# Kernel optimization log

Hardware: AMD Instinct MI355X
Metric: run time of the kernel (lower is better)

The kernel has to match this reference:

```python
import jax, jax.numpy as jnp
import numpy as np

N = 50000     # nodes
E = 800000    # edges (avg degree 16)
IN = 128
HID = 128
OUT = 128


def _init_lin(key, n_out, n_in, bias=True):
    k1, k2 = jax.random.split(key)
    bound = 1.0 / np.sqrt(n_in)
    W = jax.random.uniform(k1, (n_out, n_in), minval=-bound, maxval=bound, dtype=jnp.float32)
    if bias:
        b = jax.random.uniform(k2, (n_out,), minval=-bound, maxval=bound, dtype=jnp.float32)
        return W, b
    return W


def setup_inputs() -> dict:
    key = jax.random.key(0)
    ks = jax.random.split(key, 20)
    inp = {
        "s": jax.random.normal(ks[0], (N, IN), dtype=jnp.float32),
        "t": jax.random.normal(ks[1], (N, IN), dtype=jnp.float32),
        "edge_index": jax.random.randint(ks[2], (2, E), 0, N, dtype=jnp.int64),
        "edge_weight": jax.random.normal(ks[3], (E,), dtype=jnp.float32),
    }
    dims = [(HID, IN), (OUT, HID)]
    i = 4
    for layer in range(2):
        n_out, n_in = dims[layer]
        for pre in ("s", "t"):
            Wl, bl = _init_lin(ks[i], n_out, n_in, bias=True); i += 1
            Wr = _init_lin(ks[i], n_out, n_in, bias=False); i += 1
            inp[f"{pre}{layer}_Wl"] = Wl
            inp[f"{pre}{layer}_bl"] = bl
            inp[f"{pre}{layer}_Wr"] = Wr
    return inp


def _sage(x, src, dst, w, Wl, bl, Wr):
    """SAGEConv (mean aggr, weighted messages): lin_l(mean_j w_ij x_j) + lin_r(x_i)."""
    n = x.shape[0]
    msg = x[src] * w[:, None]                                   # [E, d] gather
    agg = jax.ops.segment_sum(msg, dst, num_segments=n)         # [N, d] scatter-add
    cnt = jax.ops.segment_sum(jnp.ones_like(w), dst, num_segments=n)
    mean = agg / jnp.maximum(cnt, 1.0)[:, None]
    return mean @ Wl.T + bl + x @ Wr.T


def reference(s, t, edge_index, edge_weight,
              s0_Wl, s0_bl, s0_Wr, t0_Wl, t0_bl, t0_Wr,
              s1_Wl, s1_bl, s1_Wr, t1_Wl, t1_bl, t1_Wr):
    w = jax.nn.sigmoid(edge_weight)
    src, dst = edge_index[0], edge_index[1]
    # layer 0 (relu; dropout is identity in eval mode)
    s1 = jax.nn.relu(_sage(t, src, dst, w, s0_Wl, s0_bl, s0_Wr))
    t1 = jax.nn.relu(_sage(s, dst, src, w, t0_Wl, t0_bl, t0_Wr))  # flipped edges
    # layer 1 (no activation)
    s2 = _sage(t1, src, dst, w, s1_Wl, s1_bl, s1_Wr)
    t2 = _sage(s1, dst, src, w, t1_Wl, t1_bl, t1_Wr)
    return (s2, t2)
```

## Files before the change

kernel.cpp:

```cpp
#include <hip/hip_runtime.h>
#include <hip/hip_bf16.h>

#define DIM 128
#define BINSHIFT 8
#define BINSZ 256
#define MAXBINS2 400
#define EPB 2048
#define CAP 6144

typedef __attribute__((ext_vector_type(4))) float f32x4;
typedef __attribute__((ext_vector_type(8))) _Float16 h16x8;
typedef __attribute__((ext_vector_type(2))) _Float16 h16x2;
typedef __attribute__((ext_vector_type(8))) unsigned short u16x8;

static __device__ __forceinline__ unsigned short f2h(float f) {
    _Float16 h = (_Float16)f;
    return __builtin_bit_cast(unsigned short, h);
}

#if __has_builtin(__builtin_amdgcn_fdot2)
static __device__ __forceinline__ float dot2(h16x2 a, h16x2 b, float c) {
    return __builtin_amdgcn_fdot2(a, b, c, false);
}
#else
static __device__ __forceinline__ float dot2(h16x2 a, h16x2 b, float c) {
    return c + (float)a.x * (float)b.x + (float)a.y * (float)b.y;
}
#endif

struct WPtrs { const float* Wl[4]; const float* Wr[4]; };

__global__ __launch_bounds__(256) void dgnn_prep(
        const float* __restrict__ s, const float* __restrict__ t,
        unsigned short* __restrict__ sb, unsigned short* __restrict__ tb,
        int n4, int cvtb, WPtrs wp, unsigned short* __restrict__ Wc, int wbase,
        int* __restrict__ binCur, int nb2) {
    int b = blockIdx.x;
    if (b < wbase) {
        int which = (b >= cvtb) ? 1 : 0;
        int i = (b - which * cvtb) * 256 + threadIdx.x;
        if (i >= n4) return;
        const float* src = which ? t : s;
        unsigned short* dst = which ? tb : sb;
        float4 v = ((const float4*)src)[i];
        ushort4 o;
        o.x = f2h(v.x); o.y = f2h(v.y); o.z = f2h(v.z); o.w = f2h(v.w);
        ((ushort4*)dst)[i] = o;
    } else if (b < wbase + 128) {
        int tid = (b - wbase) * 256 + threadIdx.x;
        int i4 = tid << 2;
        int conv = i4 >> 15;
        int rem = i4 & 32767;
        int ch = rem >> 8;
        int k = rem & 255;
        const float* src = (k < 128) ? wp.Wl[conv] : wp.Wr[conv];
        float4 v = *(const float4*)(src + ch * DIM + (k & 127));
        ushort4 o;
        o.x = f2h(v.x); o.y = f2h(v.y); o.z = f2h(v.z); o.w = f2h(v.w);
        *(ushort4*)(Wc + i4) = o;
    } else {
        for (int i = threadIdx.x; i < nb2; i += 256) binCur[i] = 0;
    }
}

__global__ __launch_bounds__(256) void dgnn_binscatter(const float* __restrict__ ew,
        const int* __restrict__ srcI, const int* __restrict__ dstI,
        int* __restrict__ binCur, int2* __restrict__ binned, int E, int NBINS) {
    __shared__ int hist[MAXBINS2];
    const int nb2 = 2 * NBINS;
    for (int i = threadIdx.x; i < nb2; i += 256) hist[i] = 0;
    __syncthreads();
    int base = blockIdx.x * EPB;
    int end = min(base + EPB, E);
    for (int e = base + threadIdx.x; e < end; e += 256) {
        atomicAdd(&hist[dstI[e] >> BINSHIFT], 1);
        atomicAdd(&hist[NBINS + (srcI[e] >> BINSHIFT)], 1);
    }
    __syncthreads();
    for (int i = threadIdx.x; i < nb2; i += 256) {
        int c = hist[i];
        int st = c ? atomicAdd(&binCur[i], c) : 0;
        hist[i] = i * CAP + st;
    }
    __syncthreads();
    for (int e = base + threadIdx.x; e < end; e += 256) {
        int d = dstI[e], s = srcI[e];
        float x = ew[e];
        float w = 1.0f / (1.0f + expf(-x));
        int wb = __float_as_int(w);
        int packed = d | (s << 16);
        int pd = atomicAdd(&hist[d >> BINSHIFT], 1);
        binned[pd] = make_int2(packed, wb);
        int ps = atomicAdd(&hist[NBINS + (s >> BINSHIFT)], 1);
        binned[ps] = make_int2(packed, wb);
    }
}

__global__ __launch_bounds__(256) void dgnn_csrfinal(const int2* __restrict__ binned,
        const int* __restrict__ binCur,
        int* __restrict__ offsD, int* __restrict__ degD,
        int* __restrict__ offsS, int* __restrict__ degS,
        unsigned int* __restrict__ nbrPD, unsigned int* __restrict__ nbrPS,
        int N, int NBINS) {
    int b = blockIdx.x;
    bool isD = b < NBINS;
    int lb = isD ? b : b - NBINS;
    int nodeBase = lb << BINSHIFT;
    const int2* bin = binned + (size_t)b * CAP;
    int K = binCur[b]; if (K > CAP) K = CAP;
    int* offs = isD ? offsD : offsS;
    int* dga  = isD ? degD : degS;
    unsigned int* out = (isD ? nbrPD : nbrPS) + (size_t)lb * CAP;

    __shared__ int cnt[BINSZ], cur[BINSZ], scanb[BINSZ];
    cnt[threadIdx.x] = 0;
    __syncthreads();
    for (int i = threadIdx.x; i < K; i += 256) {
        int pk = bin[i].x;
        int node = isD ? (pk & 0xffff) : ((pk >> 16) & 0xffff);
        atomicAdd(&cnt[node - nodeBase], 1);
    }
    __syncthreads();
    int v = cnt[threadIdx.x];
    scanb[threadIdx.x] = v;
    __syncthreads();
#pragma unroll
    for (int o = 1; o < 256; o <<= 1) {
        int u = (threadIdx.x >= o) ? scanb[threadIdx.x - o] : 0;
        __syncthreads();
        scanb[threadIdx.x] += u;
        __syncthreads();
    }
    int pos = scanb[threadIdx.x] - v;
    cur[threadIdx.x] = pos;
    int n = nodeBase + threadIdx.x;
    if (n < N) { offs[n] = lb * CAP + pos; dga[n] = v; }
    __syncthreads();
    for (int i = threadIdx.x; i < K; i += 256) {
        int2 en = bin[i];
        int node, nbr;
        if (isD) { node = en.x & 0xffff; nbr = (en.x >> 16) & 0xffff; }
        else     { node = (en.x >> 16) & 0xffff; nbr = en.x & 0xffff; }
        int p = atomicAdd(&cur[node - nodeBase], 1);
        unsigned short wh = f2h(__int_as_float(en.y));
        out[p] = (unsigned int)nbr | ((unsigned int)wh << 16);
    }
}

__global__ __launch_bounds__(256, 8) void dgnn_gather2(
        const unsigned short* __restrict__ xbD, const int* __restrict__ offsD,
        const int* __restrict__ degD, const unsigned int* __restrict__ nbrD,
        unsigned short* __restrict__ meanD,
        const unsigned short* __restrict__ xbS, const int* __restrict__ offsS,
        const int* __restrict__ degS, const unsigned int* __restrict__ nbrS,
        unsigned short* __restrict__ meanS,
        int N, int halfb) {
    int which = (blockIdx.x >= halfb) ? 1 : 0;
    const unsigned short* xb = which ? xbS : xbD;
    const int* offs          = which ? offsS : offsD;
    const int* dga           = which ? degS : degD;
    const unsigned int* nbrP = which ? nbrS : nbrD;
    unsigned short* meanb    = which ? meanS : meanD;

    long long gid = (long long)(blockIdx.x - which * halfb) * 256 + threadIdx.x;
    int n = (int)(gid >> 5);
    if (n >= N) return;
    const int l32 = (int)gid & 31;
    const int q2  = l32 >> 4;
    const int m   = l32 & 15;

    int beg = offs[n];
    int dg  = dga[n];
    int end = beg + dg;
    float acc[8];
#pragma unroll
    for (int k = 0; k < 8; k++) acc[k] = 0.f;

    for (int base = beg; base < end; base += 32) {
        int cnt = end - base; if (cnt > 32) cnt = 32;
        bool inb = (base + l32) < end;
        unsigned int pk_l = inb ? nbrP[base + l32] : 0u;

        for (int it = 0; it < cnt; it += 16) {
            int e0 = it + (q2 << 1);
            unsigned int p[8];
#pragma unroll
            for (int j = 0; j < 4; j++) {
                p[2 * j]     = __shfl(pk_l, e0 + 4 * j, 32);
                p[2 * j + 1] = __shfl(pk_l, e0 + 4 * j + 1, 32);
            }
            uint4 v[8];
#pragma unroll
            for (int j = 0; j < 8; j++)
                v[j] = *(const uint4*)(xb + ((size_t)(p[j] & 0xffffu) << 7) + (m << 3));
#pragma unroll
            for (int j = 0; j < 4; j++) {
                h16x2 wp = __builtin_bit_cast(h16x2,
                    __builtin_amdgcn_perm(p[2 * j + 1], p[2 * j], 0x07060302u));
                const unsigned int* ua = &v[2 * j].x;
                const unsigned int* ub = &v[2 * j + 1].x;
#pragma unroll
                for (int k = 0; k < 4; k++) {
                    h16x2 lo = __builtin_bit_cast(h16x2,
                        __builtin_amdgcn_perm(ub[k], ua[k], 0x05040100u));
                    h16x2 hi = __builtin_bit_cast(h16x2,
                        __builtin_amdgcn_perm(ub[k], ua[k], 0x07060302u));
                    acc[2 * k]     = dot2(wp, lo, acc[2 * k]);
                    acc[2 * k + 1] = dot2(wp, hi, acc[2 * k + 1]);
                }
            }
        }
    }

#pragma unroll
    for (int k = 0; k < 8; k++)
        acc[k] += __shfl_xor(acc[k], 16);

    if (q2 == 0) {
        float inv = 1.0f / fmaxf((float)dg, 1.0f);
        u16x8 o;
#pragma unroll
        for (int k = 0; k < 8; k++) o[k] = f2h(acc[k] * inv);
        *(u16x8*)(meanb + ((size_t)n << 7) + (m << 3)) = o;
    }
}

__global__ __launch_bounds__(256) void dgnn_node2(
        const unsigned short* __restrict__ meanA, const unsigned short* __restrict__ xbA,
        const unsigned short* __restrict__ WcA, const float* __restrict__ biasA,
        float* __restrict__ outfA, unsigned short* __restrict__ outbA,
        const unsigned short* __restrict__ meanB, const unsigned short* __restrict__ xbB,
        const unsigned short* __restrict__ WcB, const float* __restrict__ biasB,
        float* __restrict__ outfB, unsigned short* __restrict__ outbB,
        int N, int mode, int halfb) {
    __shared__ __align__(16) unsigned short sW[128 * 256];

    int which = (blockIdx.x >= halfb) ? 1 : 0;
    const unsigned short* meanb = which ? meanB : meanA;
    const unsigned short* xb    = which ? xbB : xbA;
    const unsigned short* Wc    = which ? WcB : WcA;
    const float* bias           = which ? biasB : biasA;
    float* outf                 = which ? outfB : outfA;
    unsigned short* outb        = which ? outbB : outbA;
    int lb = blockIdx.x - which * halfb;

    for (int i = threadIdx.x; i < 4096; i += 256) {
        int ch = i >> 5;
        int off = (i & 31) << 4;
        float4 v = *(const float4*)((const char*)Wc + ((size_t)i << 4));
        int soff = off ^ ((ch & 7) << 4);
        *(float4*)((char*)sW + ch * 512 + soff) = v;
    }
    __syncthreads();

    const int wid = threadIdx.x >> 6;
    const int lane = threadIdx.x & 63;
    const int r = lane & 15;
    const int q = lane >> 4;
    const int ntiles = (N + 15) >> 4;

    for (int tile = lb * 4 + wid; tile < ntiles; tile += halfb * 4) {
        const int n0 = tile << 4;
        const unsigned short* A0 = meanb + (size_t)(n0 + r) * DIM + q * 8;
        const unsigned short* A1 = xb    + (size_t)(n0 + r) * DIM + q * 8;

        f32x4 acc[8];
#pragma unroll
        for (int ct = 0; ct < 8; ct++) acc[ct] = (f32x4){0.f, 0.f, 0.f, 0.f};

#pragma unroll
        for (int ks = 0; ks < 8; ks++) {
            h16x8 a = (ks < 4) ? *(const h16x8*)(A0 + ks * 32)
                               : *(const h16x8*)(A1 + (ks - 4) * 32);
#pragma unroll
            for (int ct = 0; ct < 8; ct++) {
                int ch = ct * 16 + r;
                int soff = (ks * 64 + q * 16) ^ ((ch & 7) << 4);
                h16x8 b = *(const h16x8*)((const char*)sW + ch * 512 + soff);
                acc[ct] = __builtin_amdgcn_mfma_f32_16x16x32_f16(a, b, acc[ct], 0, 0, 0);
            }
        }

#pragma unroll
        for (int ct = 0; ct < 8; ct++) {
            int ch = ct * 16 + r;
            float bv = bias[ch];
#pragma unroll
            for (int rr = 0; rr < 4; rr++) {
                int n = n0 + q * 4 + rr;
                if (n >= N) break;
                float v = acc[ct][rr] + bv;
                if (mode) {
                    v = fmaxf(v, 0.f);
                    outb[(size_t)n * DIM + ch] = f2h(v);
                } else {
                    outf[(size_t)n * DIM + ch] = v;
                }
            }
        }
    }
}

extern "C" void kernel_launch(void* const* d_in, const int* in_sizes, int n_in,
                              void* d_out, int out_size, void* d_ws, size_t ws_size,
                              hipStream_t stream) {
    const float* s  = (const float*)d_in[0];
    const float* t  = (const float*)d_in[1];
    const int*   ei = (const int*)d_in[2];
    const float* ew = (const float*)d_in[3];
    const float* s0_Wl = (const float*)d_in[4];
    const float* s0_bl = (const float*)d_in[5];
    const float* s0_Wr = (const float*)d_in[6];
    const float* t0_Wl = (const float*)d_in[7];
    const float* t0_bl = (const float*)d_in[8];
    const float* t0_Wr = (const float*)d_in[9];
    const float* s1_Wl = (const float*)d_in[10];
    const float* s1_bl = (const float*)d_in[11];
    const float* s1_Wr = (const float*)d_in[12];
    const float* t1_Wl = (const float*)d_in[13];
    const float* t1_bl = (const float*)d_in[14];
    const float* t1_Wr = (const float*)d_in[15];

    const int N = in_sizes[0] / DIM;
    const int E = in_sizes[3];
    const int NBINS = (N + BINSZ - 1) / BINSZ;

    unsigned int* nbrPD = (unsigned int*)d_ws;
    unsigned int* nbrPS = nbrPD + (size_t)NBINS * CAP;
    unsigned short* up = (unsigned short*)(nbrPS + (size_t)NBINS * CAP);
    unsigned short* sb    = up;
    unsigned short* tb    = sb    + (size_t)N * DIM;
    unsigned short* meanA = tb    + (size_t)N * DIM;
    unsigned short* meanB = meanA + (size_t)N * DIM;
    unsigned short* s1b   = meanB + (size_t)N * DIM;
    unsigned short* t1b   = s1b   + (size_t)N * DIM;
    unsigned short* Wc    = t1b   + (size_t)N * DIM;
    int* ip     = (int*)(Wc + 4 * 128 * 256);
    int* binCur = ip;
    int* offsD  = binCur + 2 * NBINS;
    int* degD   = offsD + N;
    int* offsS  = degD + N;
    int* degS   = offsS + N;

    int2* binned = (int2*)meanA;

    float* sout = (float*)d_out;
    float* tout = sout + (size_t)N * DIM;

    const int* srcI = ei;
    const int* dstI = ei + E;

    const int binb = (E + EPB - 1) / EPB;
    const int gbH = (int)(((long long)N * 32 + 255) / 256);
    const int nodeb = 256;
    const int cvtb = ((N * DIM / 4) + 255) / 256;

    WPtrs wp;
    wp.Wl[0] = s0_Wl; wp.Wr[0] = s0_Wr;
    wp.Wl[1] = t0_Wl; wp.Wr[1] = t0_Wr;
    wp.Wl[2] = s1_Wl; wp.Wr[2] = s1_Wr;
    wp.Wl[3] = t1_Wl; wp.Wr[3] = t1_Wr;
    dgnn_prep<<<2 * cvtb + 129, 256, 0, stream>>>(s, t, sb, tb, N * DIM / 4,
                                                  cvtb, wp, Wc, 2 * cvtb,
                                                  binCur, 2 * NBINS);

    dgnn_binscatter<<<binb, 256, 0, stream>>>(ew, srcI, dstI, binCur, binned, E, NBINS);
    dgnn_csrfinal<<<2 * NBINS, 256, 0, stream>>>(binned, binCur,
                                                 offsD, degD, offsS, degS,
                                                 nbrPD, nbrPS, N, NBINS);

    dgnn_gather2<<<2 * gbH, 256, 0, stream>>>(tb, offsD, degD, nbrPD, meanA,
                                              sb, offsS, degS, nbrPS, meanB, N, gbH);
    dgnn_node2<<<2 * nodeb, 256, 0, stream>>>(
        meanA, tb, Wc,         s0_bl, nullptr, s1b,
        meanB, sb, Wc + 32768, t0_bl, nullptr, t1b, N, 1, nodeb);

    dgnn_gather2<<<2 * gbH, 256, 0, stream>>>(t1b, offsD, degD, nbrPD, meanA,
                                              s1b, offsS, degS, nbrPS, meanB, N, gbH);
    dgnn_node2<<<2 * nodeb, 256, 0, stream>>>(
        meanA, t1b, Wc + 2 * 32768, s1_bl, sout, nullptr,
        meanB, s1b, Wc + 3 * 32768, t1_bl, tout, nullptr, N, 0, nodeb);
}
```

Before: 228.2 us.

## Stage binscatter edge data in LDS and add a 4-edge tail loop to aggregation

The bin-scatter kernel now reads src/dst/weight and computes the sigmoid once, keeping the packed edge and weight in shared memory for the second pass instead of re-reading global memory and recomputing. The aggregation kernel splits its inner loop into full 16-edge chunks plus a 4-edge remainder loop, so tail iterations no longer gather 8 padded rows that contribute zero weight. This raises LDS usage per block (about 16KB), which may reduce occupancy of the binscatter kernel.

```diff
diff --git a/kernel.cpp b/kernel.cpp
--- a/kernel.cpp
+++ b/kernel.cpp
@@ -67,14 +67,23 @@
         const int* __restrict__ srcI, const int* __restrict__ dstI,
         int* __restrict__ binCur, int2* __restrict__ binned, int E, int NBINS) {
     __shared__ int hist[MAXBINS2];
+    __shared__ int epk[EPB];
+    __shared__ int ewb[EPB];
     const int nb2 = 2 * NBINS;
     for (int i = threadIdx.x; i < nb2; i += 256) hist[i] = 0;
     __syncthreads();
     int base = blockIdx.x * EPB;
     int end = min(base + EPB, E);
-    for (int e = base + threadIdx.x; e < end; e += 256) {
-        atomicAdd(&hist[dstI[e] >> BINSHIFT], 1);
-        atomicAdd(&hist[NBINS + (srcI[e] >> BINSHIFT)], 1);
+    int cnt = end - base;
+    for (int j = threadIdx.x; j < cnt; j += 256) {
+        int e = base + j;
+        int d = dstI[e], s = srcI[e];
+        float x = ew[e];
+        float w = 1.0f / (1.0f + expf(-x));
+        epk[j] = d | (s << 16);
+        ewb[j] = __float_as_int(w);
+        atomicAdd(&hist[d >> BINSHIFT], 1);
+        atomicAdd(&hist[NBINS + (s >> BINSHIFT)], 1);
     }
     __syncthreads();
     for (int i = threadIdx.x; i < nb2; i += 256) {
@@ -83,16 +92,14 @@
         hist[i] = i * CAP + st;
     }
     __syncthreads();
-    for (int e = base + threadIdx.x; e < end; e += 256) {
-        int d = dstI[e], s = srcI[e];
-        float x = ew[e];
-        float w = 1.0f / (1.0f + expf(-x));
-        int wb = __float_as_int(w);
-        int packed = d | (s << 16);
+    for (int j = threadIdx.x; j < cnt; j += 256) {
+        int pk = epk[j];
+        int wb = ewb[j];
+        int d = pk & 0xffff, s = (pk >> 16) & 0xffff;
         int pd = atomicAdd(&hist[d >> BINSHIFT], 1);
-        binned[pd] = make_int2(packed, wb);
+        binned[pd] = make_int2(pk, wb);
         int ps = atomicAdd(&hist[NBINS + (s >> BINSHIFT)], 1);
-        binned[ps] = make_int2(packed, wb);
+        binned[ps] = make_int2(pk, wb);
     }
 }
 
@@ -181,7 +188,8 @@
         bool inb = (base + l32) < end;
         unsigned int pk_l = inb ? nbrP[base + l32] : 0u;
 
-        for (int it = 0; it < cnt; it += 16) {
+        int it = 0;
+        for (; it + 16 <= cnt; it += 16) {
             int e0 = it + (q2 << 1);
             unsigned int p[8];
 #pragma unroll
@@ -208,6 +216,26 @@
                     acc[2 * k]     = dot2(wp, lo, acc[2 * k]);
                     acc[2 * k + 1] = dot2(wp, hi, acc[2 * k + 1]);
                 }
+            }
+        }
+        for (; it < cnt; it += 4) {
+            int e0 = it + (q2 << 1);
+            unsigned int pa = __shfl(pk_l, e0, 32);
+            unsigned int pb = __shfl(pk_l, e0 + 1, 32);
+            uint4 va = *(const uint4*)(xb + ((size_t)(pa & 0xffffu) << 7) + (m << 3));
+            uint4 vb = *(const uint4*)(xb + ((size_t)(pb & 0xffffu) << 7) + (m << 3));
+            h16x2 wp = __builtin_bit_cast(h16x2,
+                __builtin_amdgcn_perm(pb, pa, 0x07060302u));
+            const unsigned int* ua = &va.x;
+            const unsigned int* ub = &vb.x;
+#pragma unroll
+            for (int k = 0; k < 4; k++) {
+                h16x2 lo = __builtin_bit_cast(h16x2,
+                    __builtin_amdgcn_perm(ub[k], ua[k], 0x05040100u));
+                h16x2 hi = __builtin_bit_cast(h16x2,
+                    __builtin_amdgcn_perm(ub[k], ua[k], 0x07060302u));
+                acc[2 * k]     = dot2(wp, lo, acc[2 * k]);
+                acc[2 * k + 1] = dot2(wp, hi, acc[2 * k + 1]);
             }
         }
     }
```

Measured after the change: 227.2 us. About the same (-0.4%).
